# Kernel optimization log

Measured on AMD Instinct MI355X. Metric: run time of the kernel, lower is better.

## Reference

```python
import jax, jax.numpy as jnp
import numpy as np

MODEL_DIM = 1024
NUM_HEADS = 16
DIM_PER_HEAD = MODEL_DIM // NUM_HEADS  # 64
KERNEL = 3


def conv_causal(x, w, b):
    # x: [B, L, D_in]; w: [D_out, D_in, K]; torch Conv1d, padding=K-1, padding_mode='circular'
    xt = jnp.transpose(x, (0, 2, 1))                      # [B, D, L]
    xp = jnp.pad(xt, ((0, 0), (0, 0), (KERNEL - 1, KERNEL - 1)), mode='wrap')
    y = jax.lax.conv_general_dilated(xp, w, window_strides=(1,), padding='VALID',
                                     dimension_numbers=('NCH', 'OIH', 'NCH'))
    y = y + b[None, :, None]
    y = y[:, :, :-(KERNEL - 1)]                           # causal slice back to L
    return jax.nn.gelu(jnp.transpose(y, (0, 2, 1)), approximate=False)


def layer_norm(x, g, b, eps=1e-5):
    mu = jnp.mean(x, axis=-1, keepdims=True)
    var = jnp.var(x, axis=-1, keepdims=True)
    return (x - mu) * jax.lax.rsqrt(var + eps) * g + b


def setup_inputs() -> dict:
    key = jax.random.key(0)
    ks = jax.random.split(key, 8)
    B, L, D = 4, 1024, MODEL_DIM
    s = 0.02
    return {
        'key':   jax.random.normal(ks[0], (B, L, D), jnp.float32),
        'value': jax.random.normal(ks[1], (B, L, D), jnp.float32),
        'query': jax.random.normal(ks[2], (B, L, D), jnp.float32),
        'wk': jax.random.normal(ks[3], (D, D, KERNEL), jnp.float32) * s,
        'bk': jnp.zeros((D,), jnp.float32),
        'wv': jax.random.normal(ks[4], (D, D, KERNEL), jnp.float32) * s,
        'bv': jnp.zeros((D,), jnp.float32),
        'wq': jax.random.normal(ks[5], (D, D, KERNEL), jnp.float32) * s,
        'bq': jnp.zeros((D,), jnp.float32),
        'wf': jax.random.normal(ks[6], (D, D), jnp.float32) * s,
        'bf': jnp.zeros((D,), jnp.float32),
        'ln_g': jnp.ones((D,), jnp.float32),
        'ln_b': jnp.zeros((D,), jnp.float32),
    }


def reference(key, value, query, wk, bk, wv, bv, wq, bq, wf, bf, ln_g, ln_b):
    B = key.shape[0]
    H, d = NUM_HEADS, DIM_PER_HEAD
    residual = query
    k = conv_causal(key, wk, bk)
    v = conv_causal(value, wv, bv)
    q = conv_causal(query, wq, bq)
    # faithful row-major reshape (interleaves seq and heads, as in the torch .view)
    k = k.reshape(B * H, -1, d)
    v = v.reshape(B * H, -1, d)
    q = q.reshape(B * H, -1, d)
    scale = (d // H) ** (-0.5)  # = 0.5 for d=64, H=16 (as in source)
    attn = jnp.einsum('bqd,bkd->bqk', q, k) * scale
    attn = jnp.where(attn < 0.1, 0.1, attn)   # masked_fill_(attn < 0.1, 0.1)
    attn = jnp.log(attn)
    attn = jax.nn.log_softmax(attn, axis=-1)  # nn.LogSoftmax(dim=2)
    context = jnp.einsum('bqk,bkd->bqd', attn, v)
    context = context.reshape(B, -1, H * d)
    output = jnp.einsum('bld,od->blo', context, wf) + bf
    output = layer_norm(residual + output, ln_g, ln_b)
    return (output, attn)
```

## Files before the change

### kernel.cpp

```cpp
#include <hip/hip_runtime.h>
#include <math.h>

typedef _Float16 half8 __attribute__((ext_vector_type(8)));
typedef _Float16 half4 __attribute__((ext_vector_type(4)));
typedef float f32x4 __attribute__((ext_vector_type(4)));

#define MFMA16(a, b, c) __builtin_amdgcn_mfma_f32_16x16x32_f16(a, b, c, 0, 0, 0)

__device__ __forceinline__ void gload16(void* lds, const void* g) {
  __builtin_amdgcn_global_load_lds(
      (const __attribute__((address_space(1))) unsigned int*)g,
      (__attribute__((address_space(3))) unsigned int*)lds, 16, 0, 0);
}

__global__ __launch_bounds__(256) void cast4_kernel(
    const float* __restrict__ in, _Float16* __restrict__ out) {
  int i = blockIdx.x * 256 + threadIdx.x;
  float4 v = ((const float4*)in)[i];
  half4 h = {(_Float16)v.x, (_Float16)v.y, (_Float16)v.z, (_Float16)v.w};
  ((half4*)out)[i] = h;
}

__global__ __launch_bounds__(256) void castwt_kernel(
    const float* __restrict__ w, _Float16* __restrict__ wt) {
  int idx = blockIdx.x * 256 + threadIdx.x;
  wt[idx]           = (_Float16)w[idx * 3 + 0];
  wt[idx + 1048576] = (_Float16)w[idx * 3 + 1];
  wt[idx + 2097152] = (_Float16)w[idx * 3 + 2];
}

template <int NTAPS, bool GELU>
__global__ __launch_bounds__(256) void gemm16_kernel(
    const _Float16* __restrict__ A, const _Float16* __restrict__ Bw,
    const float* __restrict__ bias, _Float16* __restrict__ outh,
    float* __restrict__ outf) {
  __shared__ _Float16 As[64 * 64];
  __shared__ _Float16 Bs[128 * 64];
  const int t = threadIdx.x;
  const int w = t >> 6, l = t & 63;
  const int lr = l & 15, lg = l >> 4;
  const int r0 = blockIdx.x * 64, o0 = blockIdx.y * 128;
  const int l0 = r0 & 1023;
  const int wr = (w >> 1) * 32, wc = (w & 1) * 64;
  f32x4 acc[2][4];
  #pragma unroll
  for (int q = 0; q < 2; ++q)
    #pragma unroll
    for (int n = 0; n < 4; ++n) acc[q][n] = (f32x4){0.f, 0.f, 0.f, 0.f};

  const _Float16* Ab = (NTAPS == 3) ? (A + (size_t)(r0 >> 10) * 1048576) : A;

  for (int kk = 0; kk < NTAPS; ++kk) {
    const _Float16* Bb = Bw + (size_t)kk * 1048576;
    for (int i0 = 0; i0 < 1024; i0 += 64) {
      #pragma unroll
      for (int c = 0; c < 2; ++c) {
        const int idx = c * 256 + t;
        const int row = idx >> 3, c8 = (idx & 7) * 8;
        const _Float16* asrc;
        if (NTAPS == 3) {
          int ll = (l0 + row + kk - 2) & 1023;
          asrc = Ab + (size_t)ll * 1024 + i0 + c8;
        } else {
          asrc = Ab + (size_t)(r0 + row) * 1024 + i0 + c8;
        }
        gload16((char*)As + c * 4096 + w * 1024, asrc);
      }
      #pragma unroll
      for (int c = 0; c < 4; ++c) {
        const int idx = c * 256 + t;
        const int row = idx >> 3, c8 = (idx & 7) * 8;
        gload16((char*)Bs + c * 4096 + w * 1024,
                Bb + (size_t)(o0 + row) * 1024 + i0 + c8);
      }
      __syncthreads();
      half8 af[2][2];
      #pragma unroll
      for (int q = 0; q < 2; ++q)
        #pragma unroll
        for (int f = 0; f < 2; ++f)
          af[q][f] = *(const half8*)&As[(wr + q * 16 + lr) * 64 + f * 32 + lg * 8];
      #pragma unroll
      for (int n = 0; n < 4; ++n) {
        half8 bf0 = *(const half8*)&Bs[(wc + n * 16 + lr) * 64 + lg * 8];
        half8 bf1 = *(const half8*)&Bs[(wc + n * 16 + lr) * 64 + 32 + lg * 8];
        #pragma unroll
        for (int q = 0; q < 2; ++q) {
          acc[q][n] = MFMA16(af[q][0], bf0, acc[q][n]);
          acc[q][n] = MFMA16(af[q][1], bf1, acc[q][n]);
        }
      }
      __syncthreads();
    }
  }
  #pragma unroll
  for (int q = 0; q < 2; ++q) {
    const int rowb = r0 + wr + q * 16 + lg * 4;
    #pragma unroll
    for (int n = 0; n < 4; ++n) {
      const int col = o0 + wc + n * 16 + lr;
      const float bi = bias[col];
      #pragma unroll
      for (int rr = 0; rr < 4; ++rr) {
        float v = acc[q][n][rr] + bi;
        if (GELU) {
          v = 0.5f * v * (1.f + erff(v * 0.70710678118654752440f));
          outh[(size_t)(rowb + rr) * 1024 + col] = (_Float16)v;
        } else {
          outf[(size_t)(rowb + rr) * 1024 + col] = v;
        }
      }
    }
  }
}

__global__ __launch_bounds__(256) void attn_kernel(
    const _Float16* __restrict__ Qh, const _Float16* __restrict__ Kh,
    const _Float16* __restrict__ Vh, float* __restrict__ attn,
    _Float16* __restrict__ ctx) {
  __shared__ _Float16 Qs[4096];
  __shared__ _Float16 Ks[4096];
  __shared__ _Float16 VT[4096];
  __shared__ _Float16 Ps[64 * 72];
  const int t = threadIdx.x, w = t >> 6, l = t & 63;
  const int lr = l & 15, lg = l >> 4;
  const int p = blockIdx.x;
  const int q0 = blockIdx.y * 64;
  const _Float16* Qp = Qh + (size_t)p * 65536;
  const _Float16* Kp = Kh + (size_t)p * 65536;
  const _Float16* Vp = Vh + (size_t)p * 65536;

  #pragma unroll
  for (int c = 0; c < 2; ++c) {
    const int idx = c * 256 + t;
    const int row = idx >> 3;
    const int bin = ((idx & 7) * 16) ^ ((row & 7) << 4);
    gload16((char*)Qs + c * 4096 + w * 1024,
            (const char*)Qp + (size_t)(q0 + row) * 128 + bin);
  }
  __syncthreads();
  const int Rq = w * 16 + lr;
  half8 qf[2];
  #pragma unroll
  for (int f = 0; f < 2; ++f)
    qf[f] = *(const half8*)((const char*)Qs + Rq * 128 +
                            ((lg * 16 + f * 64) ^ ((Rq & 7) << 4)));

  f32x4 rs = {0.f, 0.f, 0.f, 0.f};
  for (int k0 = 0; k0 < 1024; k0 += 64) {
    #pragma unroll
    for (int c = 0; c < 2; ++c) {
      const int idx = c * 256 + t;
      const int row = idx >> 3;
      const int bin = ((idx & 7) * 16) ^ ((row & 7) << 4);
      gload16((char*)Ks + c * 4096 + w * 1024,
              (const char*)Kp + (size_t)(k0 + row) * 128 + bin);
    }
    __syncthreads();
    #pragma unroll
    for (int kj = 0; kj < 4; ++kj) {
      const int Rk = kj * 16 + lr;
      f32x4 s = {0.f, 0.f, 0.f, 0.f};
      #pragma unroll
      for (int f = 0; f < 2; ++f) {
        half8 kf = *(const half8*)((const char*)Ks + Rk * 128 +
                                   ((lg * 16 + f * 64) ^ ((Rk & 7) << 4)));
        s = MFMA16(qf[f], kf, s);
      }
      #pragma unroll
      for (int rr = 0; rr < 4; ++rr) rs[rr] += fmaxf(0.5f * s[rr], 0.1f);
    }
    __syncthreads();
  }
  #pragma unroll
  for (int m = 1; m < 16; m <<= 1) {
    #pragma unroll
    for (int rr = 0; rr < 4; ++rr) rs[rr] += __shfl_xor(rs[rr], m);
  }
  float lrs_[4];
  #pragma unroll
  for (int rr = 0; rr < 4; ++rr) lrs_[rr] = logf(rs[rr]);

  float* ao = attn + (size_t)p * 1048576 + (size_t)q0 * 1024;
  f32x4 cacc[4];
  #pragma unroll
  for (int n = 0; n < 4; ++n) cacc[n] = (f32x4){0.f, 0.f, 0.f, 0.f};

  for (int k0 = 0; k0 < 1024; k0 += 64) {
    #pragma unroll
    for (int c = 0; c < 2; ++c) {
      const int idx = c * 256 + t;
      const int row = idx >> 3;
      const int bin = ((idx & 7) * 16) ^ ((row & 7) << 4);
      gload16((char*)Ks + c * 4096 + w * 1024,
              (const char*)Kp + (size_t)(k0 + row) * 128 + bin);
    }
    #pragma unroll
    for (int u = 0; u < 4; ++u) {
      const int jg = u * 4 + w;
      half4 vv;
      #pragma unroll
      for (int jj = 0; jj < 4; ++jj)
        vv[jj] = Vp[(size_t)(k0 + jg * 4 + jj) * 64 + l];
      *(half4*)((char*)VT + l * 128 + ((jg * 8) ^ ((l & 7) << 4))) = vv;
    }
    __syncthreads();
    #pragma unroll
    for (int kj = 0; kj < 4; ++kj) {
      const int Rk = kj * 16 + lr;
      f32x4 s = {0.f, 0.f, 0.f, 0.f};
      #pragma unroll
      for (int f = 0; f < 2; ++f) {
        half8 kf = *(const half8*)((const char*)Ks + Rk * 128 +
                                   ((lg * 16 + f * 64) ^ ((Rk & 7) << 4)));
        s = MFMA16(qf[f], kf, s);
      }
      #pragma unroll
      for (int rr = 0; rr < 4; ++rr) {
        const float c_ = fmaxf(0.5f * s[rr], 0.1f);
        const float lc = logf(c_) - lrs_[rr];
        const int row = w * 16 + lg * 4 + rr;
        ao[(size_t)row * 1024 + k0 + kj * 16 + lr] = lc;
        Ps[row * 72 + kj * 16 + lr] = (_Float16)lc;
      }
    }
    __syncthreads();
    #pragma unroll
    for (int ks = 0; ks < 2; ++ks) {
      half8 pf = *(const half8*)&Ps[Rq * 72 + ks * 32 + lg * 8];
      #pragma unroll
      for (int nj = 0; nj < 4; ++nj) {
        const int dd = nj * 16 + lr;
        half8 vf = *(const half8*)((const char*)VT + dd * 128 +
                                   ((ks * 64 + lg * 16) ^ ((dd & 7) << 4)));
        cacc[nj] = MFMA16(pf, vf, cacc[nj]);
      }
    }
    __syncthreads();
  }
  #pragma unroll
  for (int nj = 0; nj < 4; ++nj) {
    const int dd = nj * 16 + lr;
    #pragma unroll
    for (int rr = 0; rr < 4; ++rr) {
      const int row = q0 + w * 16 + lg * 4 + rr;
      ctx[(size_t)p * 65536 + (size_t)row * 64 + dd] = (_Float16)cacc[nj][rr];
    }
  }
}

__global__ __launch_bounds__(256) void ln_kernel(
    const float* __restrict__ proj, const float* __restrict__ resid,
    const float* __restrict__ gam, const float* __restrict__ bet,
    float* __restrict__ out) {
  __shared__ float red[2][4];
  const int row = blockIdx.x;
  const int t = threadIdx.x;
  float4 v = ((const float4*)(proj + (size_t)row * 1024))[t];
  float4 q = ((const float4*)(resid + (size_t)row * 1024))[t];
  v.x += q.x; v.y += q.y; v.z += q.z; v.w += q.w;
  float s = v.x + v.y + v.z + v.w;
  float s2 = v.x * v.x + v.y * v.y + v.z * v.z + v.w * v.w;
  #pragma unroll
  for (int off = 32; off; off >>= 1) {
    s += __shfl_xor(s, off);
    s2 += __shfl_xor(s2, off);
  }
  const int wave = t >> 6;
  if ((t & 63) == 0) { red[0][wave] = s; red[1][wave] = s2; }
  __syncthreads();
  float S = red[0][0] + red[0][1] + red[0][2] + red[0][3];
  float S2 = red[1][0] + red[1][1] + red[1][2] + red[1][3];
  float mu = S * (1.f / 1024.f);
  float var = S2 * (1.f / 1024.f) - mu * mu;
  float inv = rsqrtf(var + 1e-5f);
  float4 gv = ((const float4*)gam)[t];
  float4 bv = ((const float4*)bet)[t];
  float4 o;
  o.x = (v.x - mu) * inv * gv.x + bv.x;
  o.y = (v.y - mu) * inv * gv.y + bv.y;
  o.z = (v.z - mu) * inv * gv.z + bv.z;
  o.w = (v.w - mu) * inv * gv.w + bv.w;
  ((float4*)out)[(size_t)row * 256 + t] = o;
}

extern "C" void kernel_launch(void* const* d_in, const int* in_sizes, int n_in,
                              void* d_out, int out_size, void* d_ws, size_t ws_size,
                              hipStream_t stream) {
  (void)in_sizes; (void)n_in; (void)out_size; (void)ws_size;
  const float* key   = (const float*)d_in[0];
  const float* value = (const float*)d_in[1];
  const float* query = (const float*)d_in[2];
  const float* wk    = (const float*)d_in[3];
  const float* bk    = (const float*)d_in[4];
  const float* wv    = (const float*)d_in[5];
  const float* bv    = (const float*)d_in[6];
  const float* wq    = (const float*)d_in[7];
  const float* bq    = (const float*)d_in[8];
  const float* wf    = (const float*)d_in[9];
  const float* bf    = (const float*)d_in[10];
  const float* ln_g  = (const float*)d_in[11];
  const float* ln_b  = (const float*)d_in[12];

  float* out  = (float*)d_out;
  float* attn = out + 4194304;

  char* ws = (char*)d_ws;
  _Float16* XB   = (_Float16*)(ws + (0u << 20));
  _Float16* WT   = (_Float16*)(ws + (8u << 20));
  _Float16* WFT  = (_Float16*)(ws + (14u << 20));
  _Float16* QF   = (_Float16*)(ws + (16u << 20));
  _Float16* KF   = (_Float16*)(ws + (24u << 20));
  _Float16* VF   = (_Float16*)(ws + (32u << 20));
  _Float16* CTX  = (_Float16*)(ws + (0u << 20));
  float*    PROJ = (float*)   (ws + (24u << 20));

  dim3 gg(64, 8);
  cast4_kernel<<<1024, 256, 0, stream>>>(wf, WFT);

  cast4_kernel<<<4096, 256, 0, stream>>>(key, XB);
  castwt_kernel<<<4096, 256, 0, stream>>>(wk, WT);
  gemm16_kernel<3, true><<<gg, 256, 0, stream>>>(XB, WT, bk, KF, nullptr);

  cast4_kernel<<<4096, 256, 0, stream>>>(value, XB);
  castwt_kernel<<<4096, 256, 0, stream>>>(wv, WT);
  gemm16_kernel<3, true><<<gg, 256, 0, stream>>>(XB, WT, bv, VF, nullptr);

  cast4_kernel<<<4096, 256, 0, stream>>>(query, XB);
  castwt_kernel<<<4096, 256, 0, stream>>>(wq, WT);
  gemm16_kernel<3, true><<<gg, 256, 0, stream>>>(XB, WT, bq, QF, nullptr);

  attn_kernel<<<dim3(64, 16), 256, 0, stream>>>(QF, KF, VF, attn, CTX);

  gemm16_kernel<1, false><<<gg, 256, 0, stream>>>(CTX, WFT, bf, nullptr, PROJ);
  ln_kernel<<<4096, 256, 0, stream>>>(PROJ, query, ln_g, ln_b, out);
}
```

Before: 644.1 us.

## Batch three conv GEMMs into one launch and swizzle GEMM LDS tiles

Merges the key/value/query casts, weight transposes and three conv GEMMs into batched launches over a z-dimension, so 512-block grids become one 1536-block grid that fills the GPU better. It also XOR-swizzles the GEMM shared-memory tiles to avoid bank conflicts on fragment reads, and pads the attention P buffer stride from 72 to 76. The cost is a larger workspace to hold all three inputs and weights at once.

After: 555.8 us. 13.7% less time.

```diff
diff --git a/kernel.cpp b/kernel.cpp
--- a/kernel.cpp
+++ b/kernel.cpp
@@ -21,16 +21,31 @@
   ((half4*)out)[i] = h;
 }
 
-__global__ __launch_bounds__(256) void castwt_kernel(
-    const float* __restrict__ w, _Float16* __restrict__ wt) {
+__global__ __launch_bounds__(256) void cast4x3_kernel(
+    const float* __restrict__ a, const float* __restrict__ b,
+    const float* __restrict__ c, _Float16* __restrict__ out) {
+  const int z = blockIdx.y;
+  const float* src = (z == 0) ? a : ((z == 1) ? b : c);
+  int i = blockIdx.x * 256 + threadIdx.x;
+  float4 v = ((const float4*)src)[i];
+  half4 h = {(_Float16)v.x, (_Float16)v.y, (_Float16)v.z, (_Float16)v.w};
+  ((half4*)(out + (size_t)z * 4194304))[i] = h;
+}
+
+__global__ __launch_bounds__(256) void castwt3_kernel(
+    const float* __restrict__ wk, const float* __restrict__ wv,
+    const float* __restrict__ wq, _Float16* __restrict__ wt) {
+  const int z = blockIdx.y;
+  const float* w = (z == 0) ? wk : ((z == 1) ? wv : wq);
+  _Float16* o = wt + (size_t)z * 3145728;
   int idx = blockIdx.x * 256 + threadIdx.x;
-  wt[idx]           = (_Float16)w[idx * 3 + 0];
-  wt[idx + 1048576] = (_Float16)w[idx * 3 + 1];
-  wt[idx + 2097152] = (_Float16)w[idx * 3 + 2];
+  o[idx]           = (_Float16)w[idx * 3 + 0];
+  o[idx + 1048576] = (_Float16)w[idx * 3 + 1];
+  o[idx + 2097152] = (_Float16)w[idx * 3 + 2];
 }
 
 template <int NTAPS, bool GELU>
-__global__ __launch_bounds__(256) void gemm16_kernel(
+__device__ __forceinline__ void gemm16_body(
     const _Float16* __restrict__ A, const _Float16* __restrict__ Bw,
     const float* __restrict__ bias, _Float16* __restrict__ outh,
     float* __restrict__ outf) {
@@ -56,34 +71,42 @@
       #pragma unroll
       for (int c = 0; c < 2; ++c) {
         const int idx = c * 256 + t;
-        const int row = idx >> 3, c8 = (idx & 7) * 8;
+        const int row = idx >> 3;
+        const int cs = ((idx & 7) ^ (row & 7)) * 8;
         const _Float16* asrc;
         if (NTAPS == 3) {
           int ll = (l0 + row + kk - 2) & 1023;
-          asrc = Ab + (size_t)ll * 1024 + i0 + c8;
+          asrc = Ab + (size_t)ll * 1024 + i0 + cs;
         } else {
-          asrc = Ab + (size_t)(r0 + row) * 1024 + i0 + c8;
+          asrc = Ab + (size_t)(r0 + row) * 1024 + i0 + cs;
         }
         gload16((char*)As + c * 4096 + w * 1024, asrc);
       }
       #pragma unroll
       for (int c = 0; c < 4; ++c) {
         const int idx = c * 256 + t;
-        const int row = idx >> 3, c8 = (idx & 7) * 8;
+        const int row = idx >> 3;
+        const int cs = ((idx & 7) ^ (row & 7)) * 8;
         gload16((char*)Bs + c * 4096 + w * 1024,
-                Bb + (size_t)(o0 + row) * 1024 + i0 + c8);
+                Bb + (size_t)(o0 + row) * 1024 + i0 + cs);
       }
       __syncthreads();
       half8 af[2][2];
       #pragma unroll
-      for (int q = 0; q < 2; ++q)
+      for (int q = 0; q < 2; ++q) {
+        const int R = wr + q * 16 + lr;
         #pragma unroll
         for (int f = 0; f < 2; ++f)
-          af[q][f] = *(const half8*)&As[(wr + q * 16 + lr) * 64 + f * 32 + lg * 8];
+          af[q][f] = *(const half8*)((const char*)As + R * 128 +
+                                     ((f * 64 + lg * 16) ^ ((R & 7) << 4)));
+      }
       #pragma unroll
       for (int n = 0; n < 4; ++n) {
-        half8 bf0 = *(const half8*)&Bs[(wc + n * 16 + lr) * 64 + lg * 8];
-        half8 bf1 = *(const half8*)&Bs[(wc + n * 16 + lr) * 64 + 32 + lg * 8];
+        const int Rb = wc + n * 16 + lr;
+        half8 bf0 = *(const half8*)((const char*)Bs + Rb * 128 +
+                                    ((lg * 16) ^ ((Rb & 7) << 4)));
+        half8 bf1 = *(const half8*)((const char*)Bs + Rb * 128 +
+                                    ((64 + lg * 16) ^ ((Rb & 7) << 4)));
         #pragma unroll
         for (int q = 0; q < 2; ++q) {
           acc[q][n] = MFMA16(af[q][0], bf0, acc[q][n]);
@@ -114,6 +137,23 @@
   }
 }
 
+__global__ __launch_bounds__(256) void conv3_kernel(
+    const _Float16* __restrict__ X3, const _Float16* __restrict__ W3,
+    const float* __restrict__ bk, const float* __restrict__ bv,
+    const float* __restrict__ bq, _Float16* __restrict__ Ko,
+    _Float16* __restrict__ Vo, _Float16* __restrict__ Qo) {
+  const int z = blockIdx.z;
+  gemm16_body<3, true>(X3 + (size_t)z * 4194304, W3 + (size_t)z * 3145728,
+                       (z == 0) ? bk : ((z == 1) ? bv : bq),
+                       (z == 0) ? Ko : ((z == 1) ? Vo : Qo), nullptr);
+}
+
+__global__ __launch_bounds__(256) void proj_kernel(
+    const _Float16* __restrict__ A, const _Float16* __restrict__ Bw,
+    const float* __restrict__ bias, float* __restrict__ outf) {
+  gemm16_body<1, false>(A, Bw, bias, nullptr, outf);
+}
+
 __global__ __launch_bounds__(256) void attn_kernel(
     const _Float16* __restrict__ Qh, const _Float16* __restrict__ Kh,
     const _Float16* __restrict__ Vh, float* __restrict__ attn,
@@ -121,7 +161,7 @@
   __shared__ _Float16 Qs[4096];
   __shared__ _Float16 Ks[4096];
   __shared__ _Float16 VT[4096];
-  __shared__ _Float16 Ps[64 * 72];
+  __shared__ _Float16 Ps[64 * 76];
   const int t = threadIdx.x, w = t >> 6, l = t & 63;
   const int lr = l & 15, lg = l >> 4;
   const int p = blockIdx.x;
@@ -221,13 +261,13 @@
         const float lc = logf(c_) - lrs_[rr];
         const int row = w * 16 + lg * 4 + rr;
         ao[(size_t)row * 1024 + k0 + kj * 16 + lr] = lc;
-        Ps[row * 72 + kj * 16 + lr] = (_Float16)lc;
+        Ps[row * 76 + kj * 16 + lr] = (_Float16)lc;
       }
     }
     __syncthreads();
     #pragma unroll
     for (int ks = 0; ks < 2; ++ks) {
-      half8 pf = *(const half8*)&Ps[Rq * 72 + ks * 32 + lg * 8];
+      half8 pf = *(const half8*)&Ps[Rq * 76 + ks * 32 + lg * 8];
       #pragma unroll
       for (int nj = 0; nj < 4; ++nj) {
         const int dd = nj * 16 + lr;
@@ -306,32 +346,24 @@
   float* attn = out + 4194304;
 
   char* ws = (char*)d_ws;
-  _Float16* XB   = (_Float16*)(ws + (0u << 20));
-  _Float16* WT   = (_Float16*)(ws + (8u << 20));
-  _Float16* WFT  = (_Float16*)(ws + (14u << 20));
-  _Float16* QF   = (_Float16*)(ws + (16u << 20));
-  _Float16* KF   = (_Float16*)(ws + (24u << 20));
-  _Float16* VF   = (_Float16*)(ws + (32u << 20));
-  _Float16* CTX  = (_Float16*)(ws + (0u << 20));
-  float*    PROJ = (float*)   (ws + (24u << 20));
-
-  dim3 gg(64, 8);
+  _Float16* XB3  = (_Float16*)(ws + ( 0ull << 20));
+  _Float16* WT3  = (_Float16*)(ws + (24ull << 20));
+  _Float16* WFT  = (_Float16*)(ws + (42ull << 20));
+  _Float16* KF   = (_Float16*)(ws + (44ull << 20));
+  _Float16* VF   = (_Float16*)(ws + (52ull << 20));
+  _Float16* QF   = (_Float16*)(ws + (60ull << 20));
+  _Float16* CTX  = (_Float16*)(ws + (68ull << 20));
+  float*    PROJ = (float*)   (ws + (76ull << 20));
+
   cast4_kernel<<<1024, 256, 0, stream>>>(wf, WFT);
-
-  cast4_kernel<<<4096, 256, 0, stream>>>(key, XB);
-  castwt_kernel<<<4096, 256, 0, stream>>>(wk, WT);
-  gemm16_kernel<3, true><<<gg, 256, 0, stream>>>(XB, WT, bk, KF, nullptr);
-
-  cast4_kernel<<<4096, 256, 0, stream>>>(value, XB);
-  castwt_kernel<<<4096, 256, 0, stream>>>(wv, WT);
-  gemm16_kernel<3, true><<<gg, 256, 0, stream>>>(XB, WT, bv, VF, nullptr);
-
-  cast4_kernel<<<4096, 256, 0, stream>>>(query, XB);
-  castwt_kernel<<<4096, 256, 0, stream>>>(wq, WT);
-  gemm16_kernel<3, true><<<gg, 256, 0, stream>>>(XB, WT, bq, QF, nullptr);
+  cast4x3_kernel<<<dim3(4096, 3), 256, 0, stream>>>(key, value, query, XB3);
+  castwt3_kernel<<<dim3(4096, 3), 256, 0, stream>>>(wk, wv, wq, WT3);
+
+  conv3_kernel<<<dim3(64, 8, 3), 256, 0, stream>>>(XB3, WT3, bk, bv, bq,
+                                                   KF, VF, QF);
 
   attn_kernel<<<dim3(64, 16), 256, 0, stream>>>(QF, KF, VF, attn, CTX);
 
-  gemm16_kernel<1, false><<<gg, 256, 0, stream>>>(CTX, WFT, bf, nullptr, PROJ);
+  proj_kernel<<<dim3(64, 8), 256, 0, stream>>>(CTX, WFT, bf, PROJ);
   ln_kernel<<<4096, 256, 0, stream>>>(PROJ, query, ln_g, ln_b, out);
 }
```
